# Kernel tuning notes

Hardware: AMD Instinct MI355X
Metric: run time of the kernel (lower is better)

## Reference

```python
import jax, jax.numpy as jnp
import numpy as np

B, S, F_IN, D, H, L, E, DFF, OUT = 16, 512, 46, 256, 8, 6, 8, 1024, 3


def _ln(x, s, b, eps=1e-5):
    m = x.mean(-1, keepdims=True)
    v = ((x - m) ** 2).mean(-1, keepdims=True)
    return (x - m) / jnp.sqrt(v + eps) * s + b


def _mha(q_in, kv_in, qkv_w, qkv_b, out_w, out_b, h):
    # torch nn.MultiheadAttention (batch_first), eval mode (no dropout)
    d = q_in.shape[-1]
    dh = d // h
    wq, wk, wv = jnp.split(qkv_w, 3, axis=0)
    bq, bk, bv = jnp.split(qkv_b, 3)
    q = (q_in @ wq.T + bq).reshape(q_in.shape[0], q_in.shape[1], h, dh)
    k = (kv_in @ wk.T + bk).reshape(kv_in.shape[0], kv_in.shape[1], h, dh)
    v = (kv_in @ wv.T + bv).reshape(kv_in.shape[0], kv_in.shape[1], h, dh)
    attn = jax.nn.softmax(jnp.einsum('bqhd,bkhd->bhqk', q, k) / jnp.sqrt(jnp.float32(dh)), axis=-1)
    o = jnp.einsum('bhqk,bkhd->bqhd', attn, v).reshape(q_in.shape[0], q_in.shape[1], d)
    return o @ out_w.T + out_b


def _moe(x, gate_w, gate_b, e_w1, e_b1, e_w2, e_b2, top_k=2):
    # Faithful to source: EVERY expert runs its dense FFN over all tokens,
    # then outputs are mixed by the top-k gate weights (zero for unrouted experts).
    logits = x @ gate_w.T + gate_b                      # (B,S,E)
    tk_logits, tk_idx = jax.lax.top_k(logits, top_k)    # (B,S,K)
    tk_probs = jax.nn.softmax(tk_logits, axis=-1)
    onehot = jax.nn.one_hot(tk_idx, logits.shape[-1], dtype=x.dtype)  # (B,S,K,E)
    weights = (onehot * tk_probs[..., None]).sum(-2)    # (B,S,E)
    hid = jax.nn.gelu(jnp.einsum('bsd,efd->bsef', x, e_w1) + e_b1, approximate=False)  # (B,S,E,DFF)
    out_e = jnp.einsum('bsef,edf->bsed', hid, e_w2) + e_b2                             # (B,S,E,D)
    out = jnp.einsum('bsed,bse->bsd', out_e, weights)
    probs = jax.nn.softmax(logits, axis=-1)
    aux = logits.shape[-1] * jnp.sum(probs.mean(axis=(0, 1)) ** 2)
    return out, aux


def _posenc(s, d):
    pos = jnp.arange(s, dtype=jnp.float32)[:, None]
    div = jnp.exp(jnp.arange(0, d, 2, dtype=jnp.float32) * (-np.log(10000.0) / d))
    pe = jnp.zeros((s, d), jnp.float32)
    pe = pe.at[:, 0::2].set(jnp.sin(pos * div)).at[:, 1::2].set(jnp.cos(pos * div))
    return pe


def _forward(x, in_w, in_b, l_qkv_w, l_qkv_b, l_out_w, l_out_b, gate_w, gate_b,
             e_w1, e_b1, e_w2, e_b2, ln1_s, ln1_b, ln2_s, ln2_b,
             p_qkv_w, p_qkv_b, p_out_w, p_out_b,
             a_w1, a_b1, a_ln1s, a_ln1b, a_w2, a_b2, a_ln2s, a_ln2b, a_w3, a_b3,
             pr_w1, pr_b1, pr_ln1s, pr_ln1b, pr_w2, pr_b2, pr_ln2s, pr_ln2b, pr_w3, pr_b3):
    h = x @ in_w.T + in_b + _posenc(x.shape[1], D)[None]
    aux_total = jnp.float32(0.0)
    # NB: source builds ModuleList([encoder_layer]*L) with the SAME instance -> shared weights
    for _ in range(L):
        attn = _mha(h, h, l_qkv_w, l_qkv_b, l_out_w, l_out_b, H)
        h = _ln(h + attn, ln1_s, ln1_b)
        moe_out, aux = _moe(h, gate_w, gate_b, e_w1, e_b1, e_w2, e_b2)
        aux_total = aux_total + aux
        h = _ln(h + moe_out, ln2_s, ln2_b)
    pooled = _mha(h[:, -1:, :], h, p_qkv_w, p_qkv_b, p_out_w, p_out_b, H)[:, 0]  # (B,D)
    # action head: Linear -> GELU -> LN -> Linear -> GELU -> LN -> Linear
    a = jax.nn.gelu(pooled @ a_w1.T + a_b1, approximate=False)
    a = _ln(a, a_ln1s, a_ln1b)
    a = jax.nn.gelu(a @ a_w2.T + a_b2, approximate=False)
    a = _ln(a, a_ln2s, a_ln2b)
    action = a @ a_w3.T + a_b3
    # profit head: Linear -> LN -> GELU -> Linear -> LN -> GELU -> Linear
    p = jax.nn.gelu(_ln(pooled @ pr_w1.T + pr_b1, pr_ln1s, pr_ln1b), approximate=False)
    p = jax.nn.gelu(_ln(p @ pr_w2.T + pr_b2, pr_ln2s, pr_ln2b), approximate=False)
    profit = p @ pr_w3.T + pr_b3
    return action, profit, aux_total


def setup_inputs() -> dict:
    key = jax.random.key(0)
    ks = iter(jax.random.split(key, 64))
    def w(shape, scale=0.02):
        return jax.random.normal(next(ks), shape, jnp.float32) * scale
    d2, d4 = D // 2, D // 4
    return dict(
        x=jax.random.normal(next(ks), (B, S, F_IN), jnp.float32),
        in_w=w((D, F_IN)), in_b=jnp.zeros(D),
        l_qkv_w=w((3 * D, D)), l_qkv_b=jnp.zeros(3 * D), l_out_w=w((D, D)), l_out_b=jnp.zeros(D),
        gate_w=w((E, D)), gate_b=jnp.zeros(E),
        e_w1=w((E, DFF, D)), e_b1=jnp.zeros((E, DFF)), e_w2=w((E, D, DFF)), e_b2=jnp.zeros((E, D)),
        ln1_s=jnp.ones(D), ln1_b=jnp.zeros(D), ln2_s=jnp.ones(D), ln2_b=jnp.zeros(D),
        p_qkv_w=w((3 * D, D)), p_qkv_b=jnp.zeros(3 * D), p_out_w=w((D, D)), p_out_b=jnp.zeros(D),
        a_w1=w((d2, D)), a_b1=jnp.zeros(d2), a_ln1s=jnp.ones(d2), a_ln1b=jnp.zeros(d2),
        a_w2=w((d4, d2)), a_b2=jnp.zeros(d4), a_ln2s=jnp.ones(d4), a_ln2b=jnp.zeros(d4),
        a_w3=w((OUT, d4)), a_b3=jnp.zeros(OUT),
        pr_w1=w((D, D)), pr_b1=jnp.zeros(D), pr_ln1s=jnp.ones(D), pr_ln1b=jnp.zeros(D),
        pr_w2=w((d2, D)), pr_b2=jnp.zeros(d2), pr_ln2s=jnp.ones(d2), pr_ln2b=jnp.zeros(d2),
        pr_w3=w((1, d2)), pr_b3=jnp.zeros(1),
    )


def reference(x, in_w, in_b, l_qkv_w, l_qkv_b, l_out_w, l_out_b, gate_w, gate_b,
              e_w1, e_b1, e_w2, e_b2, ln1_s, ln1_b, ln2_s, ln2_b,
              p_qkv_w, p_qkv_b, p_out_w, p_out_b,
              a_w1, a_b1, a_ln1s, a_ln1b, a_w2, a_b2, a_ln2s, a_ln2b, a_w3, a_b3,
              pr_w1, pr_b1, pr_ln1s, pr_ln1b, pr_w2, pr_b2, pr_ln2s, pr_ln2b, pr_w3, pr_b3):
    return _forward(x, in_w, in_b, l_qkv_w, l_qkv_b, l_out_w, l_out_b, gate_w, gate_b,
                    e_w1, e_b1, e_w2, e_b2, ln1_s, ln1_b, ln2_s, ln2_b,
                    p_qkv_w, p_qkv_b, p_out_w, p_out_b,
                    a_w1, a_b1, a_ln1s, a_ln1b, a_w2, a_b2, a_ln2s, a_ln2b, a_w3, a_b3,
                    pr_w1, pr_b1, pr_ln1s, pr_ln1b, pr_w2, pr_b2, pr_ln2s, pr_ln2b, pr_w3, pr_b3)
```

## Files before the change

### kernel.cpp

```cpp
#include <hip/hip_runtime.h>
#include <hip/hip_bf16.h>
#include <math.h>


typedef __bf16 bf16;
typedef __bf16 bf16x8 __attribute__((ext_vector_type(8)));
typedef __bf16 bf16x4 __attribute__((ext_vector_type(4)));
typedef float f32x4 __attribute__((ext_vector_type(4)));

#define NIN 41

#define GLOAD_LDS(g, l)                                                    \
    __builtin_amdgcn_global_load_lds(                                      \
        (const __attribute__((address_space(1))) void*)(g),                \
        (__attribute__((address_space(3))) void*)(l), 16, 0, 0)

struct InTab {
    const void* src[NIN];
    unsigned off[NIN];
    unsigned n[NIN];
};

__device__ __forceinline__ float gelu_exact(float x) {
    return 0.5f * x * (1.0f + erff(x * 0.70710678118654752f));
}

__global__ void sniff_kernel(const unsigned* __restrict__ xw, int* __restrict__ flag) {
    __shared__ int cnt;
    if (threadIdx.x == 0) cnt = 0;
    __syncthreads();
    const unsigned w = xw[threadIdx.x];
    const unsigned ex = (w >> 7) & 0xFFu;
    if (ex >= 107u && ex <= 133u) atomicAdd(&cnt, 1);
    __syncthreads();
    if (threadIdx.x == 0) *flag = (cnt >= 192) ? 1 : 0;
}

__global__ __launch_bounds__(256) void convert_kernel(
    InTab tab, bf16* __restrict__ dst_base, const int* __restrict__ flag) {
    const unsigned g0 = blockIdx.x * 1024u;
    int inp = 0;
#pragma unroll
    for (int i = 1; i < NIN; i++)
        if (g0 >= tab.off[i]) inp = i;
    const unsigned n = tab.n[inp];
    const unsigned i0 = g0 - tab.off[inp] + threadIdx.x * 4u;
    if (i0 >= n) return;
    const int isbf = *flag;
    bf16* dst = dst_base + tab.off[inp];
    const unsigned end = (i0 + 4u > n) ? n : i0 + 4u;
    if (isbf) {
        const unsigned short* s = (const unsigned short*)tab.src[inp];
        for (unsigned i = i0; i < end; i++) ((unsigned short*)dst)[i] = s[i];
    } else {
        const float* s = (const float*)tab.src[inp];
        for (unsigned i = i0; i < end; i++) dst[i] = (bf16)s[i];
    }
}

__global__ void out_convert_kernel(const float* __restrict__ st, void* __restrict__ out,
                                   const int* __restrict__ flag) {
    const int i = threadIdx.x;
    if (i >= 65) return;
    if (*flag) ((bf16*)out)[i] = (bf16)st[i];
    else       ((float*)out)[i] = st[i];
}

#define SWZ(r, c) (((r) * 8 + ((c) ^ ((r) & 7))) * 8)

template <int BM, int BN, int WM, int WN, bool VTOUT>
__global__ __launch_bounds__(256) void gemm_bt(
    const bf16* __restrict__ A, const bf16* __restrict__ W,
    const bf16* __restrict__ bias, bf16* __restrict__ C,
    int M, int N, int K, bf16* __restrict__ vT) {
    constexpr int BK = 64;
    __shared__ alignas(16) bf16 As[BM * BK];
    __shared__ alignas(16) bf16 Ws[BN * BK];
    const int bm0 = blockIdx.x * BM, bn0 = blockIdx.y * BN;
    const int tid = threadIdx.x;
    const int wave = tid >> 6, lane = tid & 63;
    constexpr int WCOLS = BN / WN;
    const int wm0 = (wave / WCOLS) * WM, wn0 = (wave % WCOLS) * WN;
    constexpr int MT = WM / 16, NT = WN / 16;
    f32x4 acc[MT][NT] = {};
    const int frow = lane & 15, fquad = lane >> 4;

    constexpr int AIT = BM / 32, BIT = BN / 32;
    const bf16* ag[AIT];
    const bf16* bg[BIT];
    unsigned al[AIT], bl[BIT];
#pragma unroll
    for (int i = 0; i < AIT; i++) {
        const int d = wave * (BM * 2) + i * 64 + lane;
        const int r = d >> 3, c = ((d & 7) ^ (r & 7)) * 8;
        ag[i] = A + (size_t)(bm0 + r) * K + c;
        al[i] = (unsigned)(wave * (BM * 2) + i * 64) * 8u;
    }
#pragma unroll
    for (int i = 0; i < BIT; i++) {
        const int d = wave * (BN * 2) + i * 64 + lane;
        const int r = d >> 3, c = ((d & 7) ^ (r & 7)) * 8;
        bg[i] = W + (size_t)(bn0 + r) * K + c;
        bl[i] = (unsigned)(wave * (BN * 2) + i * 64) * 8u;
    }

    for (int k0 = 0; k0 < K; k0 += BK) {
#pragma unroll
        for (int i = 0; i < AIT; i++) GLOAD_LDS(ag[i] + k0, &As[al[i]]);
#pragma unroll
        for (int i = 0; i < BIT; i++) GLOAD_LDS(bg[i] + k0, &Ws[bl[i]]);
        __syncthreads();
#pragma unroll
        for (int ks = 0; ks < BK / 32; ks++) {
            bf16x8 af[MT], bfr[NT];
#pragma unroll
            for (int mt = 0; mt < MT; mt++) {
                const int r = wm0 + mt * 16 + frow;
                af[mt] = *(const bf16x8*)&As[SWZ(r, ks * 4 + fquad)];
            }
#pragma unroll
            for (int nt = 0; nt < NT; nt++) {
                const int r = wn0 + nt * 16 + frow;
                bfr[nt] = *(const bf16x8*)&Ws[SWZ(r, ks * 4 + fquad)];
            }
#pragma unroll
            for (int mt = 0; mt < MT; mt++)
#pragma unroll
                for (int nt = 0; nt < NT; nt++)
                    acc[mt][nt] = __builtin_amdgcn_mfma_f32_16x16x32_bf16(
                        af[mt], bfr[nt], acc[mt][nt], 0, 0, 0);
        }
        __syncthreads();
    }

#pragma unroll
    for (int mt = 0; mt < MT; mt++)
#pragma unroll
        for (int nt = 0; nt < NT; nt++) {
            const int gn = bn0 + wn0 + nt * 16 + frow;
            const float bv = (float)bias[gn];
#pragma unroll
            for (int r = 0; r < 4; r++) {
                const int gm = bm0 + wm0 + mt * 16 + fquad * 4 + r;
                const float v = acc[mt][nt][r] + bv;
                if (VTOUT && gn >= 512) {
                    const int d = gn - 512;
                    const int bb = gm >> 9, s = gm & 511;
                    vT[((size_t)(bb * 8 + (d >> 5)) * 32 + (d & 31)) * 512 + s] = (bf16)v;
                } else {
                    C[(size_t)gm * N + gn] = (bf16)v;
                }
            }
        }
}

__global__ __launch_bounds__(256) void gemm_moe_w1(
    const bf16* __restrict__ A, const bf16* __restrict__ Wb,
    const bf16* __restrict__ biasb, bf16* __restrict__ hid0,
    bf16* __restrict__ hid1, const int* __restrict__ list,
    const int* __restrict__ tile_ex, const int* __restrict__ ntiles) {
    constexpr int BM = 128, BN = 128, BK = 64, WM = 64, WN = 64;
    constexpr int N = 1024, K = 256;
    const int slot = (blockIdx.x >= 71) ? 1 : 0;
    const int xi = blockIdx.x - slot * 71;
    if (xi >= ntiles[slot]) return;
    __shared__ alignas(16) bf16 As[BM * BK];
    __shared__ alignas(16) bf16 Ws[BN * BK];
    const int* mylist = list + slot * 9216;
    const int e = tile_ex[slot * 72 + xi];
    const bf16* W = Wb + (size_t)e * N * K;
    const bf16* bias = biasb + e * N;
    bf16* C = slot ? hid1 : hid0;
    const int bm0 = xi * BM, bn0 = blockIdx.y * BN;
    const int tid = threadIdx.x;
    const int wave = tid >> 6, lane = tid & 63;
    constexpr int WCOLS = BN / WN;
    const int wm0 = (wave / WCOLS) * WM, wn0 = (wave % WCOLS) * WN;
    constexpr int MT = WM / 16, NT = WN / 16;
    f32x4 acc[MT][NT] = {};
    const int frow = lane & 15, fquad = lane >> 4;

    const bf16* ag[4];
    const bf16* bg[4];
    unsigned al[4], bl[4];
#pragma unroll
    for (int i = 0; i < 4; i++) {
        const int d = wave * 256 + i * 64 + lane;
        const int r = d >> 3, c = ((d & 7) ^ (r & 7)) * 8;
        ag[i] = A + (size_t)mylist[bm0 + r] * K + c;
        al[i] = (unsigned)(wave * 256 + i * 64) * 8u;
        bg[i] = W + (size_t)(bn0 + r) * K + c;
        bl[i] = al[i];
    }

    for (int k0 = 0; k0 < K; k0 += BK) {
#pragma unroll
        for (int i = 0; i < 4; i++) GLOAD_LDS(ag[i] + k0, &As[al[i]]);
#pragma unroll
        for (int i = 0; i < 4; i++) GLOAD_LDS(bg[i] + k0, &Ws[bl[i]]);
        __syncthreads();
#pragma unroll
        for (int ks = 0; ks < 2; ks++) {
            bf16x8 af[MT], bfr[NT];
#pragma unroll
            for (int mt = 0; mt < MT; mt++) {
                const int r = wm0 + mt * 16 + frow;
                af[mt] = *(const bf16x8*)&As[SWZ(r, ks * 4 + fquad)];
            }
#pragma unroll
            for (int nt = 0; nt < NT; nt++) {
                const int r = wn0 + nt * 16 + frow;
                bfr[nt] = *(const bf16x8*)&Ws[SWZ(r, ks * 4 + fquad)];
            }
#pragma unroll
            for (int mt = 0; mt < MT; mt++)
#pragma unroll
                for (int nt = 0; nt < NT; nt++)
                    acc[mt][nt] = __builtin_amdgcn_mfma_f32_16x16x32_bf16(
                        af[mt], bfr[nt], acc[mt][nt], 0, 0, 0);
        }
        __syncthreads();
    }

#pragma unroll
    for (int mt = 0; mt < MT; mt++)
#pragma unroll
        for (int nt = 0; nt < NT; nt++) {
            const int gn = bn0 + wn0 + nt * 16 + frow;
            const float bv = (float)bias[gn];
#pragma unroll
            for (int r = 0; r < 4; r++) {
                const int gm = bm0 + wm0 + mt * 16 + fquad * 4 + r;
                C[(size_t)gm * N + gn] = (bf16)gelu_exact(acc[mt][nt][r] + bv);
            }
        }
}

__global__ __launch_bounds__(256) void gemm_moe_w2(
    const bf16* __restrict__ hid0, const bf16* __restrict__ hid1,
    const bf16* __restrict__ Wb, const bf16* __restrict__ biasb,
    bf16* __restrict__ moe0, bf16* __restrict__ moe1,
    const int* __restrict__ list, const float* __restrict__ lw,
    const int* __restrict__ tile_ex, const int* __restrict__ ntiles) {
    constexpr int BM = 128, BN = 64, BK = 64, WM = 32;
    constexpr int N = 256, K = 1024;
    const int slot = (blockIdx.x >= 71) ? 1 : 0;
    const int xi = blockIdx.x - slot * 71;
    if (xi >= ntiles[slot]) return;
    __shared__ alignas(16) bf16 As[BM * BK];
    __shared__ alignas(16) bf16 Ws[BN * BK];
    const bf16* A = slot ? hid1 : hid0;
    bf16* C = slot ? moe1 : moe0;
    const int* mylist = list + slot * 9216;
    const float* mylw = lw + slot * 9216;
    const int e = tile_ex[slot * 72 + xi];
    const bf16* W = Wb + (size_t)e * N * K;
    const bf16* bias = biasb + e * N;
    const int bm0 = xi * BM, bn0 = blockIdx.y * BN;
    const int tid = threadIdx.x;
    const int wave = tid >> 6, lane = tid & 63;
    const int wm0 = wave * WM;
    constexpr int MT = WM / 16, NT = 4;
    f32x4 acc[MT][NT] = {};
    const int frow = lane & 15, fquad = lane >> 4;

    const bf16* ag[4];
    const bf16* bg[2];
    unsigned al[4], bl[2];
#pragma unroll
    for (int i = 0; i < 4; i++) {
        const int d = wave * 256 + i * 64 + lane;
        const int r = d >> 3, c = ((d & 7) ^ (r & 7)) * 8;
        ag[i] = A + (size_t)(bm0 + r) * K + c;
        al[i] = (unsigned)(wave * 256 + i * 64) * 8u;
    }
#pragma unroll
    for (int i = 0; i < 2; i++) {
        const int d = wave * 128 + i * 64 + lane;
        const int r = d >> 3, c = ((d & 7) ^ (r & 7)) * 8;
        bg[i] = W + (size_t)(bn0 + r) * K + c;
        bl[i] = (unsigned)(wave * 128 + i * 64) * 8u;
    }

    for (int k0 = 0; k0 < K; k0 += BK) {
#pragma unroll
        for (int i = 0; i < 4; i++) GLOAD_LDS(ag[i] + k0, &As[al[i]]);
#pragma unroll
        for (int i = 0; i < 2; i++) GLOAD_LDS(bg[i] + k0, &Ws[bl[i]]);
        __syncthreads();
#pragma unroll
        for (int ks = 0; ks < 2; ks++) {
            bf16x8 af[MT], bfr[NT];
#pragma unroll
            for (int mt = 0; mt < MT; mt++) {
                const int r = wm0 + mt * 16 + frow;
                af[mt] = *(const bf16x8*)&As[SWZ(r, ks * 4 + fquad)];
            }
#pragma unroll
            for (int nt = 0; nt < NT; nt++) {
                const int r = nt * 16 + frow;
                bfr[nt] = *(const bf16x8*)&Ws[SWZ(r, ks * 4 + fquad)];
            }
#pragma unroll
            for (int mt = 0; mt < MT; mt++)
#pragma unroll
                for (int nt = 0; nt < NT; nt++)
                    acc[mt][nt] = __builtin_amdgcn_mfma_f32_16x16x32_bf16(
                        af[mt], bfr[nt], acc[mt][nt], 0, 0, 0);
        }
        __syncthreads();
    }

#pragma unroll
    for (int mt = 0; mt < MT; mt++)
#pragma unroll
        for (int nt = 0; nt < NT; nt++) {
            const int gn = bn0 + nt * 16 + frow;
            const float bv = (float)bias[gn];
#pragma unroll
            for (int r = 0; r < 4; r++) {
                const int gm = bm0 + wm0 + mt * 16 + fquad * 4 + r;
                const float v = acc[mt][nt][r] + bv;
                C[(size_t)mylist[gm] * 256 + gn] = (bf16)(mylw[gm] * v);
            }
        }
}

__global__ __launch_bounds__(256) void input_proj_kernel(
    const bf16* __restrict__ x, const bf16* __restrict__ w,
    const bf16* __restrict__ b, bf16* __restrict__ h) {
    const int m = blockIdx.x, t = threadIdx.x;
    __shared__ float xs[46];
    if (t < 46) xs[t] = (float)x[m * 46 + t];
    __syncthreads();
    float acc = (float)b[t];
#pragma unroll
    for (int k = 0; k < 46; k++) acc += xs[k] * (float)w[t * 46 + k];
    const int s = m & 511;
    const int i = t >> 1;
    const float dv = expf((float)(2 * i) * (-9.210340371976184f / 256.0f));
    const float ang = (float)s * dv;
    const float pe = (t & 1) ? cosf(ang) : sinf(ang);
    h[(size_t)m * 256 + t] = (bf16)(acc + pe);
}

__global__ __launch_bounds__(256) void ln_kernel(
    bf16* __restrict__ h, const bf16* __restrict__ a0,
    const bf16* __restrict__ a1, const bf16* __restrict__ s,
    const bf16* __restrict__ b) {
    const int m = blockIdx.x * 4 + (threadIdx.x >> 6);
    const int lane = threadIdx.x & 63;
    const int c0 = lane * 4;
    bf16x4 hv = *(const bf16x4*)&h[(size_t)m * 256 + c0];
    bf16x4 av = *(const bf16x4*)&a0[(size_t)m * 256 + c0];
    bf16x4 bv2 = *(const bf16x4*)&a1[(size_t)m * 256 + c0];
    float x[4];
    float s1 = 0.0f, s2 = 0.0f;
#pragma unroll
    for (int j = 0; j < 4; j++) {
        x[j] = (float)hv[j] + (float)av[j] + (float)bv2[j];
        s1 += x[j];
        s2 += x[j] * x[j];
    }
#pragma unroll
    for (int msk = 1; msk < 64; msk <<= 1) {
        s1 += __shfl_xor(s1, msk, 64);
        s2 += __shfl_xor(s2, msk, 64);
    }
    const float mean = s1 * (1.0f / 256.0f);
    const float var = fmaxf(s2 * (1.0f / 256.0f) - mean * mean, 0.0f);
    const float inv = rsqrtf(var + 1e-5f);
    bf16x4 sv = *(const bf16x4*)&s[c0];
    bf16x4 bv = *(const bf16x4*)&b[c0];
    bf16x4 o;
#pragma unroll
    for (int j = 0; j < 4; j++)
        o[j] = (bf16)((x[j] - mean) * inv * (float)sv[j] + (float)bv[j]);
    *(bf16x4*)&h[(size_t)m * 256 + c0] = o;
}

__global__ __launch_bounds__(256) void gate_ln_kernel(
    bf16* __restrict__ h, const bf16* __restrict__ addv,
    const bf16* __restrict__ lns, const bf16* __restrict__ lnb,
    const bf16* __restrict__ gw, const bf16* __restrict__ gb,
    int* __restrict__ top_e, float* __restrict__ top_w,
    int* __restrict__ g_hist, float* __restrict__ aux_sums) {
    __shared__ alignas(16) bf16 hs[128][264];
    __shared__ alignas(16) bf16 gws[8][264];
    __shared__ float lg[128][9];
    __shared__ float mxs[128], invs[128];
    __shared__ int hist[16];
    const int tid = threadIdx.x;
    {
        const int e = tid >> 5, k = (tid & 31) * 8;
        *(bf16x8*)&gws[e][k] = *(const bf16x8*)&gw[e * 256 + k];
    }
    if (tid < 16) hist[tid] = 0;

    const int tl = tid >> 1, half = tid & 1;
    const int tok = blockIdx.x * 128 + tl;
    const int c0 = half * 128;
    float s1 = 0.0f, s2 = 0.0f;
#pragma unroll
    for (int j = 0; j < 128; j += 8) {
        bf16x8 hv = *(const bf16x8*)&h[(size_t)tok * 256 + c0 + j];
        bf16x8 av = *(const bf16x8*)&addv[(size_t)tok * 256 + c0 + j];
        bf16x8 xw;
#pragma unroll
        for (int q = 0; q < 8; q++) {
            const float xq = (float)hv[q] + (float)av[q];
            xw[q] = (bf16)xq;
            s1 += xq;
            s2 += xq * xq;
        }
        *(bf16x8*)&hs[tl][c0 + j] = xw;
    }
    s1 += __shfl_xor(s1, 1, 64);
    s2 += __shfl_xor(s2, 1, 64);
    const float mean = s1 * (1.0f / 256.0f);
    const float var = fmaxf(s2 * (1.0f / 256.0f) - mean * mean, 0.0f);
    const float inv = rsqrtf(var + 1e-5f);
#pragma unroll
    for (int j = 0; j < 128; j += 8) {
        bf16x8 xw = *(const bf16x8*)&hs[tl][c0 + j];
        bf16x8 sv = *(const bf16x8*)&lns[c0 + j];
        bf16x8 bv = *(const bf16x8*)&lnb[c0 + j];
        bf16x8 o;
#pragma unroll
        for (int q = 0; q < 8; q++)
            o[q] = (bf16)(((float)xw[q] - mean) * inv * (float)sv[q] + (float)bv[q]);
        *(bf16x8*)&hs[tl][c0 + j] = o;
        *(bf16x8*)&h[(size_t)tok * 256 + c0 + j] = o;
    }
    __syncthreads();

    const int e = tid & 7;
#pragma unroll
    for (int pass = 0; pass < 4; pass++) {
        const int t2 = pass * 32 + (tid >> 3);
        float acc = 0.0f;
        for (int k = 0; k < 256; k += 8) {
            bf16x8 hv = *(const bf16x8*)&hs[t2][k];
            bf16x8 wv = *(const bf16x8*)&gws[e][k];
#pragma unroll
            for (int q = 0; q < 8; q++) acc += (float)hv[q] * (float)wv[q];
        }
        lg[t2][e] = acc + (float)gb[e];
    }
    __syncthreads();

    if (tid < 128) {
        const int t2 = blockIdx.x * 128 + tid;
        float l[8];
#pragma unroll
        for (int j = 0; j < 8; j++) l[j] = lg[tid][j];
        int i0 = 0;
#pragma unroll
        for (int j = 1; j < 8; j++)
            if (l[j] > l[i0]) i0 = j;
        int i1 = -1;
#pragma unroll
        for (int j = 0; j < 8; j++)
            if (j != i0 && (i1 < 0 || l[j] > l[i1])) i1 = j;
        const float p0 = 1.0f / (1.0f + expf(l[i1] - l[i0]));
        top_e[t2] = i0;         top_w[t2] = p0;
        top_e[8192 + t2] = i1;  top_w[8192 + t2] = 1.0f - p0;
        atomicAdd(&hist[i0], 1);
        atomicAdd(&hist[8 + i1], 1);
        const float mx = l[i0];
        float se = 0.0f;
#pragma unroll
        for (int j = 0; j < 8; j++) se += expf(l[j] - mx);
        mxs[tid] = mx;
        invs[tid] = 1.0f / se;
    }
    __syncthreads();
    if (tid < 8) {
        float s = 0.0f;
        for (int t = 0; t < 128; t++) s += expf(lg[t][tid] - mxs[t]) * invs[t];
        atomicAdd(&aux_sums[tid], s);
    }
    if (tid < 16) g_hist[blockIdx.x * 16 + tid] = hist[tid];
}

__global__ __launch_bounds__(256) void scatter_route_kernel(
    const int* __restrict__ g_hist, const int* __restrict__ top_e,
    const float* __restrict__ top_w, int* __restrict__ ntiles,
    int* __restrict__ tile_ex, int* __restrict__ list, float* __restrict__ lw) {
    __shared__ int gh[64][16];
    __shared__ int s_cnt[16], s_pre[16], s_off[16], pos[16];
    const int tid = threadIdx.x;
    for (int i = tid; i < 1024; i += 256) gh[i >> 4][i & 15] = g_hist[i];
    __syncthreads();
    if (tid < 16) {
        int run = 0, pre = 0;
        for (int b = 0; b < 64; b++) {
            if (b == (int)blockIdx.x) pre = run;
            run += gh[b][tid];
        }
        s_cnt[tid] = run;
        s_pre[tid] = pre;
    }
    __syncthreads();
    if (tid < 2) {
        const int slot = tid;
        int o = 0;
        for (int e2 = 0; e2 < 8; e2++) {
            s_off[slot * 8 + e2] = o;
            const int nt = (s_cnt[slot * 8 + e2] + 127) >> 7;
            if (blockIdx.x == 0)
                for (int t = 0; t < nt; t++) tile_ex[slot * 72 + (o >> 7) + t] = e2;
            o += nt << 7;
        }
        if (blockIdx.x == 0) ntiles[slot] = o >> 7;
    }
    __syncthreads();
    if (tid < 16) pos[tid] = s_off[tid] + s_pre[tid];
    __syncthreads();
    if (blockIdx.x == 0) {
        for (int idx = tid; idx < 16 * 128; idx += 256) {
            const int seg = idx >> 7, i = idx & 127;
            const int slot = seg >> 3;
            const int start = s_off[seg] + s_cnt[seg];
            const int end = s_off[seg] + ((s_cnt[seg] + 127) & ~127);
            const int p = start + i;
            if (p < end) {
                list[slot * 9216 + p] = 8192;
                lw[slot * 9216 + p] = 0.0f;
            }
        }
    }
    if (tid < 128) {
        const int tok = blockIdx.x * 128 + tid;
#pragma unroll
        for (int slot = 0; slot < 2; slot++) {
            const int e = top_e[slot * 8192 + tok];
            const float w = top_w[slot * 8192 + tok];
            const int idx = atomicAdd(&pos[slot * 8 + e], 1);
            list[slot * 9216 + idx] = tok;
            lw[slot * 9216 + idx] = w;
        }
    }
}

__global__ __launch_bounds__(256) void attn_kernel(
    const bf16* __restrict__ qkv, const bf16* __restrict__ vT,
    bf16* __restrict__ aout) {
    __shared__ alignas(16) bf16 P[32][520];
    __shared__ float wsum[4][32];
    __shared__ float sinv[32];
    const int s0 = blockIdx.x * 32;
    const int b = blockIdx.y >> 3, hh = blockIdx.y & 7;
    const int tid = threadIdx.x, wave = tid >> 6, lane = tid & 63;
    const int frow = lane & 15, fquad = lane >> 4;
    const size_t base = (size_t)b * 512;
    const float CST = 0.25505654f;

    bf16x8 qf[2];
#pragma unroll
    for (int mt = 0; mt < 2; mt++)
        qf[mt] = *(const bf16x8*)&qkv[(base + s0 + mt * 16 + frow) * 768 + hh * 32 + fquad * 8];
    float rsum[2][4] = {};
#pragma unroll
    for (int k8 = 0; k8 < 8; k8++) {
        const int key0 = (wave * 8 + k8) * 16;
        bf16x8 kf = *(const bf16x8*)&qkv[(base + key0 + frow) * 768 + 256 + hh * 32 + fquad * 8];
#pragma unroll
        for (int mt = 0; mt < 2; mt++) {
            f32x4 c = {};
            c = __builtin_amdgcn_mfma_f32_16x16x32_bf16(qf[mt], kf, c, 0, 0, 0);
#pragma unroll
            for (int r = 0; r < 4; r++) {
                const float e_ = __builtin_exp2f(fminf(c[r] * CST, 60.0f));
                P[mt * 16 + fquad * 4 + r][key0 + frow] = (bf16)e_;
                rsum[mt][r] += e_;
            }
        }
    }
#pragma unroll
    for (int mt = 0; mt < 2; mt++)
#pragma unroll
        for (int r = 0; r < 4; r++) {
#pragma unroll
            for (int m = 1; m < 16; m <<= 1)
                rsum[mt][r] += __shfl_xor(rsum[mt][r], m, 64);
        }
    if (frow == 0) {
#pragma unroll
        for (int mt = 0; mt < 2; mt++)
#pragma unroll
            for (int r = 0; r < 4; r++)
                wsum[wave][mt * 16 + fquad * 4 + r] = rsum[mt][r];
    }
    __syncthreads();
    if (tid < 32)
        sinv[tid] = 1.0f / (wsum[0][tid] + wsum[1][tid] + wsum[2][tid] + wsum[3][tid]);

    {
        const int mt = wave >> 1, nt = wave & 1;
        const bf16* vrow = &vT[((size_t)(b * 8 + hh) * 32 + nt * 16 + frow) * 512];
        f32x4 o = {};
#pragma unroll
        for (int ks = 0; ks < 16; ks++) {
            bf16x8 pf = *(const bf16x8*)&P[mt * 16 + frow][ks * 32 + fquad * 8];
            bf16x8 vf = *(const bf16x8*)&vrow[ks * 32 + fquad * 8];
            o = __builtin_amdgcn_mfma_f32_16x16x32_bf16(pf, vf, o, 0, 0, 0);
        }
        __syncthreads();
        const int r0 = mt * 16 + fquad * 4;
#pragma unroll
        for (int r = 0; r < 4; r++)
            aout[(base + s0 + r0 + r) * 256 + hh * 32 + nt * 16 + frow] =
                (bf16)(o[r] * sinv[r0 + r]);
    }
}

__global__ __launch_bounds__(256) void pooled_attn_kernel(
    const bf16* __restrict__ qkv, const bf16* __restrict__ vT,
    bf16* __restrict__ pa) {
    const int wid = blockIdx.x * 4 + (threadIdx.x >> 6);
    const int lane = threadIdx.x & 63;
    const int b = wid >> 3, hh = wid & 7;
    const size_t base = (size_t)b * 512;
    const float scale = 0.17677669529663687f;
    float q[32];
// ... 71 lines not shown

    auto block_ln = [&](float* v, int W, const bf16* ls, const bf16* lb) {
        const float val = (t < W) ? v[t] : 0.0f;
        r1[t] = val;
        r2[t] = val * val;
        __syncthreads();
        for (int off = 128; off > 0; off >>= 1) {
            if (t < off) { r1[t] += r1[t + off]; r2[t] += r2[t + off]; }
            __syncthreads();
        }
        const float mean = r1[0] / (float)W;
        const float var = fmaxf(r2[0] / (float)W - mean * mean, 0.0f);
        const float inv = rsqrtf(var + 1e-5f);
        __syncthreads();
        if (t < W) v[t] = (val - mean) * inv * (float)ls[t] + (float)lb[t];
        __syncthreads();
    };

    float a;
    if (t < 128) {
        a = (float)ab1[t];
        for (int k = 0; k < 256; k++) a += pool[k] * (float)aw1[t * 256 + k];
        buf[t] = gelu_exact(a);
    }
    __syncthreads();
    block_ln(buf, 128, aln1s, aln1b);
    if (t < 64) {
        a = (float)ab2[t];
        for (int k = 0; k < 128; k++) a += buf[k] * (float)aw2[t * 128 + k];
        buf2[t] = gelu_exact(a);
    }
    __syncthreads();
    block_ln(buf2, 64, aln2s, aln2b);
    if (t < 3) {
        a = (float)ab3[t];
        for (int k = 0; k < 64; k++) a += buf2[k] * (float)aw3[t * 64 + k];
        out[b * 3 + t] = a;
    }

    a = (float)pb1[t];
    for (int k = 0; k < 256; k++) a += pool[k] * (float)pw1[t * 256 + k];
    buf[t] = a;
    __syncthreads();
    block_ln(buf, 256, pln1s, pln1b);
    buf[t] = gelu_exact(buf[t]);
    __syncthreads();
    if (t < 128) {
        a = (float)pb2[t];
        for (int k = 0; k < 256; k++) a += buf[k] * (float)pw2[t * 256 + k];
        buf2[t] = a;
    }
    __syncthreads();
    block_ln(buf2, 128, pln2s, pln2b);
    if (t < 128) buf2[t] = gelu_exact(buf2[t]);
    __syncthreads();
    if (t == 0) {
        a = (float)pb3[0];
        for (int k = 0; k < 128; k++) a += buf2[k] * (float)pw3[k];
        out[48 + b] = a;
    }
}

__global__ void aux_kernel(const float* __restrict__ sums, float* __restrict__ out) {
    if (threadIdx.x == 0 && blockIdx.x == 0) {
        float tot = 0.0f;
        for (int l = 0; l < 6; l++)
            for (int e = 0; e < 8; e++) {
                const float mn = sums[l * 8 + e] * (1.0f / 8192.0f);
                tot += 8.0f * mn * mn;
            }
        out[64] = tot;
    }
}

extern "C" void kernel_launch(void* const* d_in, const int* in_sizes, int n_in,
                              void* d_out, int out_size, void* d_ws, size_t ws_size,
                              hipStream_t stream) {
    char* ws = (char*)d_ws;
    const size_t MB = 1024 * 1024;
    bf16*  h     = (bf16*)(ws);
    bf16*  moe0  = (bf16*)(ws + 8 * MB);
    bf16*  moe1  = (bf16*)(ws + 13 * MB);
    char*  ctrl  = ws + 20 * MB;
    float* auxs   = (float*)(ctrl + 0);
    int*   flag   = (int*)(ctrl + 192);
    int*   ntiles = (int*)(ctrl + 256);
    int*   tileex = (int*)(ctrl + 320);
    float* ostage = (float*)(ctrl + 1024);
    int*   g_hist = (int*)(ctrl + 2048);
    int*   top_e  = (int*)(ctrl + 10240);
    float* top_w  = (float*)(ctrl + 75776);
    int*   list   = (int*)(ctrl + 141312);
    float* lw     = (float*)(ctrl + 215040);
    bf16*  qkv   = (bf16*)(ws + 24 * MB);
    bf16*  aoutb = (bf16*)(ws + 40 * MB);
    bf16*  projo = (bf16*)(ws + 48 * MB);
    bf16*  hid0  = (bf16*)(ws + 56 * MB);
    bf16*  hid1  = (bf16*)(ws + 80 * MB);
    bf16*  vT    = (bf16*)(ws + 104 * MB);
    bf16*  pattn  = (bf16*)(ws + 110 * MB);
    bf16*  pooled = (bf16*)(ws + 110 * MB + 8192);
    bf16*  cvbase = (bf16*)(ws + 112 * MB);

    InTab tab;
    unsigned off = 0;
    bf16* cv[NIN];
    for (int i = 0; i < NIN; i++) {
        tab.src[i] = d_in[i];
        tab.off[i] = off;
        tab.n[i] = (unsigned)in_sizes[i];
        cv[i] = cvbase + off;
        off += ((unsigned)in_sizes[i] + 1023u) & ~1023u;
    }
    const int cv_blocks = (int)(off >> 10);

    const bf16 *x = cv[0], *in_w = cv[1], *in_b = cv[2], *qkv_w = cv[3], *qkv_b = cv[4],
               *out_w = cv[5], *out_b = cv[6], *gate_w = cv[7], *gate_b = cv[8],
               *e_w1 = cv[9], *e_b1 = cv[10], *e_w2 = cv[11], *e_b2 = cv[12],
               *ln1_s = cv[13], *ln1_b = cv[14], *ln2_s = cv[15], *ln2_b = cv[16],
               *pqkv_w = cv[17], *pqkv_b = cv[18], *pout_w = cv[19], *pout_b = cv[20],
               *a_w1 = cv[21], *a_b1 = cv[22], *a_ln1s = cv[23], *a_ln1b = cv[24],
               *a_w2 = cv[25], *a_b2 = cv[26], *a_ln2s = cv[27], *a_ln2b = cv[28],
               *a_w3 = cv[29], *a_b3 = cv[30],
               *pr_w1 = cv[31], *pr_b1 = cv[32], *pr_ln1s = cv[33], *pr_ln1b = cv[34],
               *pr_w2 = cv[35], *pr_b2 = cv[36], *pr_ln2s = cv[37], *pr_ln2b = cv[38],
               *pr_w3 = cv[39], *pr_b3 = cv[40];

    sniff_kernel<<<1, 256, 0, stream>>>((const unsigned*)d_in[0], flag);
    convert_kernel<<<cv_blocks, 256, 0, stream>>>(tab, cvbase, flag);

    hipMemsetAsync(auxs, 0, 192, stream);
    input_proj_kernel<<<8192, 256, 0, stream>>>(x, in_w, in_b, h);

    for (int l = 0; l < 6; l++) {
        gemm_bt<64, 128, 32, 64, true><<<dim3(128, 6), 256, 0, stream>>>(
            h, qkv_w, qkv_b, qkv, 8192, 768, 256, vT);
        attn_kernel<<<dim3(16, 128), 256, 0, stream>>>(qkv, vT, aoutb);
        gemm_bt<64, 64, 32, 32, false><<<dim3(128, 4), 256, 0, stream>>>(
            aoutb, out_w, out_b, projo, 8192, 256, 256, vT);
        gate_ln_kernel<<<64, 256, 0, stream>>>(h, projo, ln1_s, ln1_b,
                                               gate_w, gate_b,
                                               top_e, top_w, g_hist, auxs + l * 8);
        scatter_route_kernel<<<64, 256, 0, stream>>>(g_hist, top_e, top_w,
                                                     ntiles, tileex, list, lw);
        gemm_moe_w1<<<dim3(142, 8), 256, 0, stream>>>(
            h, e_w1, e_b1, hid0, hid1, list, tileex, ntiles);
        gemm_moe_w2<<<dim3(142, 4), 256, 0, stream>>>(
            hid0, hid1, e_w2, e_b2, moe0, moe1, list, lw, tileex, ntiles);
        ln_kernel<<<2048, 256, 0, stream>>>(h, moe0, moe1, ln2_s, ln2_b);
    }

    gemm_bt<64, 128, 32, 64, true><<<dim3(128, 6), 256, 0, stream>>>(
        h, pqkv_w, pqkv_b, qkv, 8192, 768, 256, vT);
    pooled_attn_kernel<<<32, 256, 0, stream>>>(qkv, vT, pattn);
    pooled_proj_kernel<<<16, 256, 0, stream>>>(pattn, pout_w, pout_b, pooled);

    heads_kernel<<<16, 256, 0, stream>>>(
        pooled,
        a_w1, a_b1, a_ln1s, a_ln1b, a_w2, a_b2, a_ln2s, a_ln2b, a_w3, a_b3,
        pr_w1, pr_b1, pr_ln1s, pr_ln1b, pr_w2, pr_b2, pr_ln2s, pr_ln2b, pr_w3, pr_b3,
        ostage);
    aux_kernel<<<1, 64, 0, stream>>>(auxs, ostage);
    out_convert_kernel<<<1, 128, 0, stream>>>(ostage, d_out, flag);
}
```

Measured before the change: 1.086 ms.

## Fuse attention out-projection with residual LayerNorm and MoE gating

Replaces the separate out-projection GEMM and gate/LayerNorm kernel with a single kernel. Each block computes a 32x256 tile of the projection, adds bias and residual, applies LayerNorm, writes h, and computes gate logits, top-2 routing and aux probabilities in place. This removes the projo intermediate round trip and one launch per layer. The aux sums now go through per-block partials that the routing kernel reduces instead of global atomics, and the routing kernel is resized to 256 blocks. In exchange, each fused block reloads the full 256x256 weight and runs only 256 blocks, which may lower GEMM efficiency.

New measurement: 1.096 ms (median of 2 runs). No clear change (+1.0%).

```diff
diff --git a/kernel.cpp b/kernel.cpp
--- a/kernel.cpp
+++ b/kernel.cpp
@@ -14,6 +14,8 @@
     __builtin_amdgcn_global_load_lds(                                      \
         (const __attribute__((address_space(1))) void*)(g),                \
         (__attribute__((address_space(3))) void*)(l), 16, 0, 0)
+
+#define SWZ(r, c) (((r) * 8 + ((c) ^ ((r) & 7))) * 8)
 
 struct InTab {
     const void* src[NIN];
@@ -65,8 +67,6 @@
     if (*flag) ((bf16*)out)[i] = (bf16)st[i];
     else       ((float*)out)[i] = st[i];
 }
-
-#define SWZ(r, c) (((r) * 8 + ((c) ^ ((r) & 7))) * 8)
 
 template <int BM, int BN, int WM, int WN, bool VTOUT>
 __global__ __launch_bounds__(256) void gemm_bt(
@@ -114,15 +114,11 @@
         for (int ks = 0; ks < BK / 32; ks++) {
             bf16x8 af[MT], bfr[NT];
 #pragma unroll
-            for (int mt = 0; mt < MT; mt++) {
-                const int r = wm0 + mt * 16 + frow;
-                af[mt] = *(const bf16x8*)&As[SWZ(r, ks * 4 + fquad)];
-            }
-#pragma unroll
-            for (int nt = 0; nt < NT; nt++) {
-                const int r = wn0 + nt * 16 + frow;
-                bfr[nt] = *(const bf16x8*)&Ws[SWZ(r, ks * 4 + fquad)];
-            }
+            for (int mt = 0; mt < MT; mt++)
+                af[mt] = *(const bf16x8*)&As[SWZ(wm0 + mt * 16 + frow, ks * 4 + fquad)];
+#pragma unroll
+            for (int nt = 0; nt < NT; nt++)
+                bfr[nt] = *(const bf16x8*)&Ws[SWZ(wn0 + nt * 16 + frow, ks * 4 + fquad)];
 #pragma unroll
             for (int mt = 0; mt < MT; mt++)
 #pragma unroll
@@ -152,6 +148,258 @@
                 }
             }
         }
+}
+
+__global__ __launch_bounds__(256) void outproj_gate_kernel(
+    const bf16* __restrict__ A,
+    const bf16* __restrict__ W,
+    const bf16* __restrict__ obias,
+    bf16* __restrict__ h,
+    const bf16* __restrict__ lns, const bf16* __restrict__ lnb,
+    const bf16* __restrict__ gw, const bf16* __restrict__ gb,
+    int* __restrict__ top_e, float* __restrict__ top_w,
+    int* __restrict__ g_hist, float* __restrict__ auxpart) {
+    constexpr int BK = 64, K = 256;
+    __shared__ alignas(16) char smem[40960];
+    bf16* As = (bf16*)smem;
+    bf16* Ws = (bf16*)(smem + 4096);
+    bf16* gws = (bf16*)smem;
+    float* red = (float*)(smem + 36864);
+    float* lgred = (float*)(smem + 37376);
+    int* hist = (int*)(smem + 39424);
+    float* auxl = (float*)(smem + 39488);
+    const int tid = threadIdx.x;
+    const int wave = tid >> 6, lane = tid & 63;
+    const int frow = lane & 15, fquad = lane >> 4;
+    const int wm0 = (wave >> 1) * 16, wn0 = (wave & 1) * 128;
+    const int bm0 = blockIdx.x * 32;
+    f32x4 acc[8] = {};
+
+    const bf16* ag;
+    unsigned al;
+    {
+        const int d = wave * 64 + lane;
+        const int r = d >> 3, c = ((d & 7) ^ (r & 7)) * 8;
+        ag = A + (size_t)(bm0 + r) * K + c;
+        al = (unsigned)(wave * 64) * 8u;
+    }
+    const bf16* bg[8];
+    unsigned bl[8];
+#pragma unroll
+    for (int i = 0; i < 8; i++) {
+        const int d = wave * 512 + i * 64 + lane;
+        const int r = d >> 3, c = ((d & 7) ^ (r & 7)) * 8;
+        bg[i] = W + (size_t)r * K + c;
+        bl[i] = (unsigned)(wave * 512 + i * 64) * 8u;
+    }
+
+    for (int k0 = 0; k0 < K; k0 += BK) {
+        GLOAD_LDS(ag + k0, &As[al]);
+#pragma unroll
+        for (int i = 0; i < 8; i++) GLOAD_LDS(bg[i] + k0, &Ws[bl[i]]);
+        __syncthreads();
+#pragma unroll
+        for (int ks = 0; ks < 2; ks++) {
+            bf16x8 af = *(const bf16x8*)&As[SWZ(wm0 + frow, ks * 4 + fquad)];
+#pragma unroll
+            for (int nt = 0; nt < 8; nt++) {
+                bf16x8 bfr = *(const bf16x8*)&Ws[SWZ(wn0 + nt * 16 + frow, ks * 4 + fquad)];
+                acc[nt] = __builtin_amdgcn_mfma_f32_16x16x32_bf16(af, bfr, acc[nt], 0, 0, 0);
+            }
+        }
+        __syncthreads();
+    }
+
+    {
+        const int e = tid >> 5, k = (tid & 31) * 8;
+        *(bf16x8*)&gws[e * 256 + k] = *(const bf16x8*)&gw[e * 256 + k];
+    }
+    if (tid < 16) hist[tid] = 0;
+    if (tid < 8) auxl[tid] = 0.0f;
+
+    float val[8][4];
+    float s1[4] = {0.f, 0.f, 0.f, 0.f}, s2[4] = {0.f, 0.f, 0.f, 0.f};
+#pragma unroll
+    for (int nt = 0; nt < 8; nt++) {
+        const int gn = wn0 + nt * 16 + frow;
+        const float bv = (float)obias[gn];
+#pragma unroll
+        for (int r = 0; r < 4; r++) {
+            const int gm = bm0 + wm0 + fquad * 4 + r;
+            const float v = acc[nt][r] + bv + (float)h[(size_t)gm * 256 + gn];
+            val[nt][r] = v;
+            s1[r] += v;
+            s2[r] += v * v;
+        }
+    }
+#pragma unroll
+    for (int r = 0; r < 4; r++) {
+#pragma unroll
+        for (int m = 1; m < 16; m <<= 1) {
+            s1[r] += __shfl_xor(s1[r], m, 64);
+            s2[r] += __shfl_xor(s2[r], m, 64);
+        }
+    }
+    if (frow == 0) {
+#pragma unroll
+        for (int r = 0; r < 4; r++) {
+            const int row = wm0 + fquad * 4 + r;
+            red[(row * 2 + (wave & 1)) * 2 + 0] = s1[r];
+            red[(row * 2 + (wave & 1)) * 2 + 1] = s2[r];
+        }
+    }
+    __syncthreads();
+
+    float lp[8][4];
+#pragma unroll
+    for (int e = 0; e < 8; e++)
+#pragma unroll
+        for (int r = 0; r < 4; r++) lp[e][r] = 0.0f;
+#pragma unroll
+    for (int r = 0; r < 4; r++) {
+        const int row = wm0 + fquad * 4 + r;
+        const float t1 = red[(row * 2 + 0) * 2 + 0] + red[(row * 2 + 1) * 2 + 0];
+        const float t2 = red[(row * 2 + 0) * 2 + 1] + red[(row * 2 + 1) * 2 + 1];
+        const float mean = t1 * (1.0f / 256.0f);
+        const float var = fmaxf(t2 * (1.0f / 256.0f) - mean * mean, 0.0f);
+        const float inv = rsqrtf(var + 1e-5f);
+#pragma unroll
+        for (int nt = 0; nt < 8; nt++) {
+            const int gn = wn0 + nt * 16 + frow;
+            const float hn = (val[nt][r] - mean) * inv * (float)lns[gn] + (float)lnb[gn];
+            h[(size_t)(bm0 + row) * 256 + gn] = (bf16)hn;
+            val[nt][r] = hn;
+        }
+    }
+#pragma unroll
+    for (int nt = 0; nt < 8; nt++) {
+        const int gn = wn0 + nt * 16 + frow;
+#pragma unroll
+        for (int e = 0; e < 8; e++) {
+            const float wv = (float)gws[e * 256 + gn];
+#pragma unroll
+            for (int r = 0; r < 4; r++) lp[e][r] += val[nt][r] * wv;
+        }
+    }
+#pragma unroll
+    for (int e = 0; e < 8; e++)
+#pragma unroll
+        for (int r = 0; r < 4; r++) {
+#pragma unroll
+            for (int m = 1; m < 16; m <<= 1)
+                lp[e][r] += __shfl_xor(lp[e][r], m, 64);
+        }
+    if (frow == 0) {
+#pragma unroll
+        for (int r = 0; r < 4; r++) {
+            const int row = wm0 + fquad * 4 + r;
+#pragma unroll
+            for (int e = 0; e < 8; e++)
+                lgred[(row * 2 + (wave & 1)) * 8 + e] = lp[e][r];
+        }
+    }
+    __syncthreads();
+
+    if ((wave & 1) == 0 && frow == 0) {
+#pragma unroll
+        for (int r = 0; r < 4; r++) {
+            const int row = wm0 + fquad * 4 + r;
+            const int tok = bm0 + row;
+            float l[8];
+#pragma unroll
+            for (int e = 0; e < 8; e++)
+                l[e] = lgred[(row * 2 + 0) * 8 + e] + lgred[(row * 2 + 1) * 8 + e] + (float)gb[e];
+            int i0 = 0;
+#pragma unroll
+            for (int j = 1; j < 8; j++)
+                if (l[j] > l[i0]) i0 = j;
+            int i1 = -1;
+#pragma unroll
+            for (int j = 0; j < 8; j++)
+                if (j != i0 && (i1 < 0 || l[j] > l[i1])) i1 = j;
+            const float p0 = 1.0f / (1.0f + expf(l[i1] - l[i0]));
+            top_e[tok] = i0;         top_w[tok] = p0;
+            top_e[8192 + tok] = i1;  top_w[8192 + tok] = 1.0f - p0;
+            atomicAdd(&hist[i0], 1);
+            atomicAdd(&hist[8 + i1], 1);
+            const float mx = l[i0];
+            float se = 0.0f, pe[8];
+#pragma unroll
+            for (int j = 0; j < 8; j++) { pe[j] = expf(l[j] - mx); se += pe[j]; }
+            const float sinv = 1.0f / se;
+#pragma unroll
+            for (int j = 0; j < 8; j++) atomicAdd(&auxl[j], pe[j] * sinv);
+        }
+    }
+    __syncthreads();
+    if (tid < 16) g_hist[blockIdx.x * 16 + tid] = hist[tid];
+    if (tid < 8) auxpart[blockIdx.x * 8 + tid] = auxl[tid];
+}
+
+__global__ __launch_bounds__(256) void scatter_route_kernel(
+    const int* __restrict__ g_hist, const float* __restrict__ auxpart,
+    const int* __restrict__ top_e, const float* __restrict__ top_w,
+    int* __restrict__ ntiles, int* __restrict__ tile_ex,
+    int* __restrict__ list, float* __restrict__ lw, float* __restrict__ auxs) {
+    __shared__ int gh[256 * 16];
+    __shared__ int s_cnt[16], s_pre[16], s_off[16], pos[16];
+    const int tid = threadIdx.x;
+    for (int i = tid; i < 4096; i += 256) gh[i] = g_hist[i];
+    __syncthreads();
+    if (tid < 16) {
+        int run = 0, pre = 0;
+        for (int b = 0; b < 256; b++) {
+            if (b == (int)blockIdx.x) pre = run;
+            run += gh[b * 16 + tid];
+        }
+        s_cnt[tid] = run;
+        s_pre[tid] = pre;
+    }
+    __syncthreads();
+    if (tid < 2) {
+        const int slot = tid;
+        int o = 0;
+        for (int e2 = 0; e2 < 8; e2++) {
+            s_off[slot * 8 + e2] = o;
+            const int nt = (s_cnt[slot * 8 + e2] + 127) >> 7;
+            if (blockIdx.x == 0)
+                for (int t = 0; t < nt; t++) tile_ex[slot * 72 + (o >> 7) + t] = e2;
+            o += nt << 7;
+        }
+        if (blockIdx.x == 0) ntiles[slot] = o >> 7;
+    }
+    __syncthreads();
+    if (tid < 16) pos[tid] = s_off[tid] + s_pre[tid];
+    __syncthreads();
+    if (blockIdx.x == 0) {
+        for (int idx = tid; idx < 2048; idx += 256) {
+            const int seg = idx >> 7, i = idx & 127;
+            const int slot = seg >> 3;
+            const int start = s_off[seg] + s_cnt[seg];
+            const int end = s_off[seg] + ((s_cnt[seg] + 127) & ~127);
+            const int p = start + i;
+            if (p < end) {
+                list[slot * 9216 + p] = 8192;
+                lw[slot * 9216 + p] = 0.0f;
+            }
+        }
+        if (tid < 8) {
+            float s = 0.0f;
+            for (int b = 0; b < 256; b++) s += auxpart[b * 8 + tid];
+            auxs[tid] = s;
+        }
+    }
+    if (tid < 32) {
+        const int tok = blockIdx.x * 32 + tid;
+#pragma unroll
+        for (int slot = 0; slot < 2; slot++) {
+            const int e = top_e[slot * 8192 + tok];
+            const float w = top_w[slot * 8192 + tok];
+            const int idx = atomicAdd(&pos[slot * 8 + e], 1);
+            list[slot * 9216 + idx] = tok;
+            lw[slot * 9216 + idx] = w;
+        }
+    }
 }
 
 __global__ __launch_bounds__(256) void gemm_moe_w1(
@@ -174,15 +422,14 @@
     const int bm0 = xi * BM, bn0 = blockIdx.y * BN;
     const int tid = threadIdx.x;
     const int wave = tid >> 6, lane = tid & 63;
-    constexpr int WCOLS = BN / WN;
-    const int wm0 = (wave / WCOLS) * WM, wn0 = (wave % WCOLS) * WN;
+    const int wm0 = (wave >> 1) * WM, wn0 = (wave & 1) * WN;
     constexpr int MT = WM / 16, NT = WN / 16;
     f32x4 acc[MT][NT] = {};
     const int frow = lane & 15, fquad = lane >> 4;
 
     const bf16* ag[4];
     const bf16* bg[4];
-    unsigned al[4], bl[4];
+    unsigned al[4];
 #pragma unroll
     for (int i = 0; i < 4; i++) {
         const int d = wave * 256 + i * 64 + lane;
@@ -190,28 +437,23 @@
         ag[i] = A + (size_t)mylist[bm0 + r] * K + c;
         al[i] = (unsigned)(wave * 256 + i * 64) * 8u;
         bg[i] = W + (size_t)(bn0 + r) * K + c;
-        bl[i] = al[i];
     }
 
     for (int k0 = 0; k0 < K; k0 += BK) {
 #pragma unroll
         for (int i = 0; i < 4; i++) GLOAD_LDS(ag[i] + k0, &As[al[i]]);
 #pragma unroll
-        for (int i = 0; i < 4; i++) GLOAD_LDS(bg[i] + k0, &Ws[bl[i]]);
+        for (int i = 0; i < 4; i++) GLOAD_LDS(bg[i] + k0, &Ws[al[i]]);
         __syncthreads();
 #pragma unroll
         for (int ks = 0; ks < 2; ks++) {
             bf16x8 af[MT], bfr[NT];
 #pragma unroll
-            for (int mt = 0; mt < MT; mt++) {
-                const int r = wm0 + mt * 16 + frow;
-                af[mt] = *(const bf16x8*)&As[SWZ(r, ks * 4 + fquad)];
-            }
-#pragma unroll
-            for (int nt = 0; nt < NT; nt++) {
-                const int r = wn0 + nt * 16 + frow;
-                bfr[nt] = *(const bf16x8*)&Ws[SWZ(r, ks * 4 + fquad)];
-            }
+            for (int mt = 0; mt < MT; mt++)
+                af[mt] = *(const bf16x8*)&As[SWZ(wm0 + mt * 16 + frow, ks * 4 + fquad)];
+#pragma unroll
+            for (int nt = 0; nt < NT; nt++)
+                bfr[nt] = *(const bf16x8*)&Ws[SWZ(wn0 + nt * 16 + frow, ks * 4 + fquad)];
 #pragma unroll
             for (int mt = 0; mt < MT; mt++)
 #pragma unroll
@@ -292,15 +534,11 @@
         for (int ks = 0; ks < 2; ks++) {
             bf16x8 af[MT], bfr[NT];
 #pragma unroll
-            for (int mt = 0; mt < MT; mt++) {
-                const int r = wm0 + mt * 16 + frow;
-                af[mt] = *(const bf16x8*)&As[SWZ(r, ks * 4 + fquad)];
-            }
-#pragma unroll
-            for (int nt = 0; nt < NT; nt++) {
-                const int r = nt * 16 + frow;
-                bfr[nt] = *(const bf16x8*)&Ws[SWZ(r, ks * 4 + fquad)];
-            }
+            for (int mt = 0; mt < MT; mt++)
+                af[mt] = *(const bf16x8*)&As[SWZ(wm0 + mt * 16 + frow, ks * 4 + fquad)];
+#pragma unroll
+            for (int nt = 0; nt < NT; nt++)
+                bfr[nt] = *(const bf16x8*)&Ws[SWZ(nt * 16 + frow, ks * 4 + fquad)];
 #pragma unroll
             for (int mt = 0; mt < MT; mt++)
 #pragma unroll
@@ -377,170 +615,6 @@
     for (int j = 0; j < 4; j++)
         o[j] = (bf16)((x[j] - mean) * inv * (float)sv[j] + (float)bv[j]);
     *(bf16x4*)&h[(size_t)m * 256 + c0] = o;
-}
-
-__global__ __launch_bounds__(256) void gate_ln_kernel(
-    bf16* __restrict__ h, const bf16* __restrict__ addv,
-    const bf16* __restrict__ lns, const bf16* __restrict__ lnb,
-    const bf16* __restrict__ gw, const bf16* __restrict__ gb,
-    int* __restrict__ top_e, float* __restrict__ top_w,
-    int* __restrict__ g_hist, float* __restrict__ aux_sums) {
-    __shared__ alignas(16) bf16 hs[128][264];
-    __shared__ alignas(16) bf16 gws[8][264];
-    __shared__ float lg[128][9];
-    __shared__ float mxs[128], invs[128];
-    __shared__ int hist[16];
-    const int tid = threadIdx.x;
-    {
-        const int e = tid >> 5, k = (tid & 31) * 8;
-        *(bf16x8*)&gws[e][k] = *(const bf16x8*)&gw[e * 256 + k];
-    }
-    if (tid < 16) hist[tid] = 0;
-
-    const int tl = tid >> 1, half = tid & 1;
-    const int tok = blockIdx.x * 128 + tl;
-    const int c0 = half * 128;
-    float s1 = 0.0f, s2 = 0.0f;
-#pragma unroll
-    for (int j = 0; j < 128; j += 8) {
-        bf16x8 hv = *(const bf16x8*)&h[(size_t)tok * 256 + c0 + j];
-        bf16x8 av = *(const bf16x8*)&addv[(size_t)tok * 256 + c0 + j];
-        bf16x8 xw;
-#pragma unroll
-        for (int q = 0; q < 8; q++) {
-            const float xq = (float)hv[q] + (float)av[q];
-            xw[q] = (bf16)xq;
-            s1 += xq;
-            s2 += xq * xq;
-        }
-        *(bf16x8*)&hs[tl][c0 + j] = xw;
-    }
-    s1 += __shfl_xor(s1, 1, 64);
-    s2 += __shfl_xor(s2, 1, 64);
-    const float mean = s1 * (1.0f / 256.0f);
-    const float var = fmaxf(s2 * (1.0f / 256.0f) - mean * mean, 0.0f);
-    const float inv = rsqrtf(var + 1e-5f);
-#pragma unroll
-    for (int j = 0; j < 128; j += 8) {
-        bf16x8 xw = *(const bf16x8*)&hs[tl][c0 + j];
-        bf16x8 sv = *(const bf16x8*)&lns[c0 + j];
-        bf16x8 bv = *(const bf16x8*)&lnb[c0 + j];
-        bf16x8 o;
-#pragma unroll
-        for (int q = 0; q < 8; q++)
-            o[q] = (bf16)(((float)xw[q] - mean) * inv * (float)sv[q] + (float)bv[q]);
-        *(bf16x8*)&hs[tl][c0 + j] = o;
-        *(bf16x8*)&h[(size_t)tok * 256 + c0 + j] = o;
-    }
-    __syncthreads();
-
-    const int e = tid & 7;
-#pragma unroll
-    for (int pass = 0; pass < 4; pass++) {
-        const int t2 = pass * 32 + (tid >> 3);
-        float acc = 0.0f;
-        for (int k = 0; k < 256; k += 8) {
-            bf16x8 hv = *(const bf16x8*)&hs[t2][k];
-            bf16x8 wv = *(const bf16x8*)&gws[e][k];
-#pragma unroll
-            for (int q = 0; q < 8; q++) acc += (float)hv[q] * (float)wv[q];
-        }
-        lg[t2][e] = acc + (float)gb[e];
-    }
-    __syncthreads();
-
-    if (tid < 128) {
-        const int t2 = blockIdx.x * 128 + tid;
-        float l[8];
-#pragma unroll
-        for (int j = 0; j < 8; j++) l[j] = lg[tid][j];
-        int i0 = 0;
-#pragma unroll
-        for (int j = 1; j < 8; j++)
-            if (l[j] > l[i0]) i0 = j;
-        int i1 = -1;
-#pragma unroll
-        for (int j = 0; j < 8; j++)
-            if (j != i0 && (i1 < 0 || l[j] > l[i1])) i1 = j;
-        const float p0 = 1.0f / (1.0f + expf(l[i1] - l[i0]));
-        top_e[t2] = i0;         top_w[t2] = p0;
-        top_e[8192 + t2] = i1;  top_w[8192 + t2] = 1.0f - p0;
-        atomicAdd(&hist[i0], 1);
-        atomicAdd(&hist[8 + i1], 1);
-        const float mx = l[i0];
-        float se = 0.0f;
-#pragma unroll
-        for (int j = 0; j < 8; j++) se += expf(l[j] - mx);
-        mxs[tid] = mx;
-        invs[tid] = 1.0f / se;
-    }
-    __syncthreads();
-    if (tid < 8) {
-        float s = 0.0f;
-        for (int t = 0; t < 128; t++) s += expf(lg[t][tid] - mxs[t]) * invs[t];
-        atomicAdd(&aux_sums[tid], s);
-    }
-    if (tid < 16) g_hist[blockIdx.x * 16 + tid] = hist[tid];
-}
-
-__global__ __launch_bounds__(256) void scatter_route_kernel(
-    const int* __restrict__ g_hist, const int* __restrict__ top_e,
-    const float* __restrict__ top_w, int* __restrict__ ntiles,
-    int* __restrict__ tile_ex, int* __restrict__ list, float* __restrict__ lw) {
-    __shared__ int gh[64][16];
-    __shared__ int s_cnt[16], s_pre[16], s_off[16], pos[16];
-    const int tid = threadIdx.x;
-    for (int i = tid; i < 1024; i += 256) gh[i >> 4][i & 15] = g_hist[i];
-    __syncthreads();
-    if (tid < 16) {
-        int run = 0, pre = 0;
-        for (int b = 0; b < 64; b++) {
-            if (b == (int)blockIdx.x) pre = run;
-            run += gh[b][tid];
-        }
-        s_cnt[tid] = run;
-        s_pre[tid] = pre;
-    }
-    __syncthreads();
-    if (tid < 2) {
-        const int slot = tid;
-        int o = 0;
-        for (int e2 = 0; e2 < 8; e2++) {
-            s_off[slot * 8 + e2] = o;
-            const int nt = (s_cnt[slot * 8 + e2] + 127) >> 7;
-            if (blockIdx.x == 0)
-                for (int t = 0; t < nt; t++) tile_ex[slot * 72 + (o >> 7) + t] = e2;
-            o += nt << 7;
-        }
-        if (blockIdx.x == 0) ntiles[slot] = o >> 7;
-    }
-    __syncthreads();
-    if (tid < 16) pos[tid] = s_off[tid] + s_pre[tid];
-    __syncthreads();
-    if (blockIdx.x == 0) {
-        for (int idx = tid; idx < 16 * 128; idx += 256) {
-            const int seg = idx >> 7, i = idx & 127;
-            const int slot = seg >> 3;
-            const int start = s_off[seg] + s_cnt[seg];
-            const int end = s_off[seg] + ((s_cnt[seg] + 127) & ~127);
-            const int p = start + i;
-            if (p < end) {
-                list[slot * 9216 + p] = 8192;
-                lw[slot * 9216 + p] = 0.0f;
-            }
-        }
-    }
-    if (tid < 128) {
-        const int tok = blockIdx.x * 128 + tid;
-#pragma unroll
-        for (int slot = 0; slot < 2; slot++) {
-            const int e = top_e[slot * 8192 + tok];
-            const float w = top_w[slot * 8192 + tok];
-            const int idx = atomicAdd(&pos[slot * 8 + e], 1);
-            list[slot * 9216 + idx] = tok;
-            lw[slot * 9216 + idx] = w;
-        }
-    }
 }
 
 __global__ __launch_bounds__(256) void attn_kernel(
@@ -778,19 +852,19 @@
     bf16*  moe0  = (bf16*)(ws + 8 * MB);
     bf16*  moe1  = (bf16*)(ws + 13 * MB);
     char*  ctrl  = ws + 20 * MB;
-    float* auxs   = (float*)(ctrl + 0);
-    int*   flag   = (int*)(ctrl + 192);
-    int*   ntiles = (int*)(ctrl + 256);
-    int*   tileex = (int*)(ctrl + 320);
-    float* ostage = (float*)(ctrl + 1024);
-    int*   g_hist = (int*)(ctrl + 2048);
-    int*   top_e  = (int*)(ctrl + 10240);
-    float* top_w  = (float*)(ctrl + 75776);
-    int*   list   = (int*)(ctrl + 141312);
-    float* lw     = (float*)(ctrl + 215040);
+    float* auxs    = (float*)(ctrl + 0);
+    int*   flag    = (int*)(ctrl + 192);
+    int*   ntiles  = (int*)(ctrl + 256);
+    int*   tileex  = (int*)(ctrl + 320);
+    float* ostage  = (float*)(ctrl + 1024);
+    int*   g_hist  = (int*)(ctrl + 2048);
+    float* auxpart = (float*)(ctrl + 18432);
+    int*   top_e   = (int*)(ctrl + 26624);
+    float* top_w   = (float*)(ctrl + 92160);
+    int*   list    = (int*)(ctrl + 157696);
+    float* lw      = (float*)(ctrl + 231424);
     bf16*  qkv   = (bf16*)(ws + 24 * MB);
     bf16*  aoutb = (bf16*)(ws + 40 * MB);
-    bf16*  projo = (bf16*)(ws + 48 * MB);
     bf16*  hid0  = (bf16*)(ws + 56 * MB);
     bf16*  hid1  = (bf16*)(ws + 80 * MB);
     bf16*  vT    = (bf16*)(ws + 104 * MB);
@@ -832,13 +906,11 @@
         gemm_bt<64, 128, 32, 64, true><<<dim3(128, 6), 256, 0, stream>>>(
             h, qkv_w, qkv_b, qkv, 8192, 768, 256, vT);
         attn_kernel<<<dim3(16, 128), 256, 0, stream>>>(qkv, vT, aoutb);
-        gemm_bt<64, 64, 32, 32, false><<<dim3(128, 4), 256, 0, stream>>>(
-            aoutb, out_w, out_b, projo, 8192, 256, 256, vT);
-        gate_ln_kernel<<<64, 256, 0, stream>>>(h, projo, ln1_s, ln1_b,
-                                               gate_w, gate_b,
-                                               top_e, top_w, g_hist, auxs + l * 8);
-        scatter_route_kernel<<<64, 256, 0, stream>>>(g_hist, top_e, top_w,
-                                                     ntiles, tileex, list, lw);
+        outproj_gate_kernel<<<256, 256, 0, stream>>>(
+            aoutb, out_w, out_b, h, ln1_s, ln1_b, gate_w, gate_b,
+            top_e, top_w, g_hist, auxpart);
+        scatter_route_kernel<<<256, 256, 0, stream>>>(
+            g_hist, auxpart, top_e, top_w, ntiles, tileex, list, lw, auxs + l * 8);
         gemm_moe_w1<<<dim3(142, 8), 256, 0, stream>>>(
             h, e_w1, e_b1, hid0, hid1, list, tileex, ntiles);
         gemm_moe_w2<<<dim3(142, 4), 256, 0, stream>>>(
```
